# Optimization experiments

Measured on AMD Instinct MI355X. Metric: run time of the kernel, lower is better.

## Reference

```python
import jax, jax.numpy as jnp
import numpy as np

B, N, Q, H = 32, 1024, 64, 768


def setup_inputs() -> dict:
    key = jax.random.key(0)
    k1, k2, k3, k4 = jax.random.split(key, 4)
    return {
        "nodes_compress": jax.random.normal(k1, (B, N, H), dtype=jnp.float32),
        "query_compress": jax.random.normal(k2, (B, Q, H), dtype=jnp.float32),
        "nodes_hidden": jax.random.normal(k3, (B, N, H), dtype=jnp.float32),
        # nn.Linear(3H, 1, bias=False).weight flattened to (3H,)
        "w": jax.random.normal(k4, (3 * H,), dtype=jnp.float32) * (1.0 / np.sqrt(3 * H)),
    }


def reference(nodes_compress, query_compress, nodes_hidden, w):
    h = nodes_compress.shape[-1]
    w_n, w_q, w_nq = w[:h], w[h:2 * h], w[2 * h:]
    # Decomposed trilinear similarity: identical to Linear([n, q, n*q]) -> scalar
    sim = (
        (nodes_compress @ w_n)[:, :, None]          # (B, N, 1)
        + (query_compress @ w_q)[:, None, :]        # (B, 1, Q)
        + jnp.einsum("bnh,bqh,h->bnq", nodes_compress, query_compress, w_nq)
    )                                                # (B, N, Q)
    # nodes -> query attention
    a = jax.nn.softmax(sim, axis=-1)                 # (B, N, Q)
    nodes2query = jnp.einsum("bnq,bqh->bnh", a, query_compress)
    # query -> nodes attention (max over query, softmax over nodes)
    b = jax.nn.softmax(jnp.max(sim, axis=-1), axis=-1)  # (B, N)
    q2n = jnp.einsum("bn,bnh->bh", b, nodes_compress)[:, None, :]  # (B, 1, H)
    q2n = jnp.broadcast_to(q2n, nodes_compress.shape)               # (B, N, H)
    return jnp.concatenate(
        [nodes_compress, nodes2query, nodes_compress * nodes2query, nodes_compress * q2n],
        axis=-1,
    )  # (B, N, 4H)
```

## Files before the change

kernel.cpp:

```cpp
#include <hip/hip_runtime.h>
#include <hip/hip_bf16.h>

#define BB 32
#define NN 1024
#define QQ 64
#define HH 768

typedef __attribute__((ext_vector_type(8))) short short8;
typedef __attribute__((ext_vector_type(4))) float f32x4;

#define GLOAD_LDS16(gp, lp) \
  __builtin_amdgcn_global_load_lds((const __attribute__((address_space(1))) unsigned int*)(gp), \
                                   (__attribute__((address_space(3))) unsigned int*)(lp), 16, 0, 0)

__device__ __forceinline__ unsigned short f2b(float f) {
  unsigned int u = __float_as_uint(f);
  unsigned int r = u + 0x7fffu + ((u >> 16) & 1u);
  return (unsigned short)(r >> 16);
}

__global__ __launch_bounds__(256) void k_prep(
    const float* __restrict__ qc, const float* __restrict__ w,
    unsigned short* __restrict__ qwB, unsigned short* __restrict__ qcT,
    float* __restrict__ sq_part) {
  __shared__ float qcL[128][66];

  const int tid = threadIdx.x;
  const int bid = blockIdx.x;
  const int b = bid / 6, hc = bid % 6;
  const float* qcB = qc + (size_t)(b * 64) * HH + hc * 128;

#pragma unroll
  for (int i = 0; i < 8; ++i) {
    int u = i * 256 + tid;
    int q = u >> 5, c4 = u & 31;
    float4 v = *(const float4*)(qcB + (size_t)q * HH + c4 * 4);
    qcL[c4 * 4 + 0][q] = v.x;
    qcL[c4 * 4 + 1][q] = v.y;
    qcL[c4 * 4 + 2][q] = v.z;
    qcL[c4 * 4 + 3][q] = v.w;
  }
  __syncthreads();

  {
    char* dst = (char*)qwB + ((size_t)bid << 14);
#pragma unroll
    for (int i = 0; i < 4; ++i) {
      int p = i * 256 + tid;
      int q = p >> 4, uu = p & 15;
      int hg = hc * 128 + uu * 8;
      short8 v;
#pragma unroll
      for (int j = 0; j < 8; ++j)
        v[j] = (short)f2b(qcL[uu * 8 + j][q] * w[2 * HH + hg + j] + w[hg + j]);
      *(short8*)(dst + ((size_t)(q * 16 + (uu ^ (q & 7)))) * 16) = v;
    }
  }
  {
    char* dst = (char*)qcT + ((size_t)bid << 14);
#pragma unroll
    for (int i = 0; i < 4; ++i) {
      int p = i * 256 + tid;
      int r = p >> 3, x = p & 7;
      int xu = x ^ (r & 7);
      short8 v;
#pragma unroll
      for (int j = 0; j < 8; ++j) v[j] = (short)f2b(qcL[r][xu * 8 + j]);
      *(short8*)(dst + (size_t)p * 16) = v;
    }
  }
  {
    int q = tid >> 2, qt = tid & 3;
    float s = 0.f;
#pragma unroll
    for (int k = 0; k < 32; ++k)
      s += qcL[qt * 32 + k][q] * w[HH + hc * 128 + qt * 32 + k];
    s += __shfl_xor(s, 1);
    s += __shfl_xor(s, 2);
    if (qt == 0) sq_part[bid * 64 + q] = s;
  }
}

__global__ __launch_bounds__(256) void k_sim(
    const float* __restrict__ nc, const unsigned short* __restrict__ qwB,
    const float* __restrict__ sq_part, float* __restrict__ partial,
    float* __restrict__ mtse, unsigned short* __restrict__ probs)
{
  __shared__ __align__(16) char bbuf[2][16384];
  __shared__ float rowmF[64];
  __shared__ float wvF[64];
  __shared__ float pW[4][768];

  const int tid = threadIdx.x;
  const int wv_ = tid >> 6, l = tid & 63;
  const int l15 = l & 15, lg = l >> 4;
  const int lb = (blockIdx.x & 7) * 64 + (blockIdx.x >> 3);
  const int b = lb >> 4, tile = lb & 15;
  const int row0 = tile * 64;

  const float* ncB = nc + (size_t)(b * NN + row0) * HH;
  const char* qwb = (const char*)qwB + (size_t)b * 98304;
  const float* aBase = ncB + (wv_ * 16 + l15) * HH + lg * 8;

  {
    const char* gsrc = qwb + wv_ * 4096 + l * 16;
#pragma unroll
    for (int i = 0; i < 4; ++i)
      GLOAD_LDS16(gsrc + i * 1024, &bbuf[0][wv_ * 4096 + i * 1024]);
  }
  float4 fr[2][8];
#pragma unroll
  for (int ks = 0; ks < 4; ++ks) {
    fr[0][ks * 2]     = *(const float4*)(aBase + ks * 32);
    fr[0][ks * 2 + 1] = *(const float4*)(aBase + ks * 32 + 4);
  }

  f32x4 acc[4] = {};
#pragma unroll
  for (int kc = 0; kc < 6; ++kc) {
    short8 af[4];
#pragma unroll
    for (int ks = 0; ks < 4; ++ks) {
      float4 f0 = fr[kc & 1][ks * 2], f1 = fr[kc & 1][ks * 2 + 1];
      short8 v;
      v[0] = (short)f2b(f0.x); v[1] = (short)f2b(f0.y);
      v[2] = (short)f2b(f0.z); v[3] = (short)f2b(f0.w);
      v[4] = (short)f2b(f1.x); v[5] = (short)f2b(f1.y);
      v[6] = (short)f2b(f1.z); v[7] = (short)f2b(f1.w);
      af[ks] = v;
    }
    if (kc < 5) {
#pragma unroll
      for (int ks = 0; ks < 4; ++ks) {
        fr[(kc + 1) & 1][ks * 2]     = *(const float4*)(aBase + (kc + 1) * 128 + ks * 32);
        fr[(kc + 1) & 1][ks * 2 + 1] = *(const float4*)(aBase + (kc + 1) * 128 + ks * 32 + 4);
      }
      const char* gsrc = qwb + (kc + 1) * 16384 + wv_ * 4096 + l * 16;
#pragma unroll
      for (int i = 0; i < 4; ++i)
        GLOAD_LDS16(gsrc + i * 1024, &bbuf[(kc + 1) & 1][wv_ * 4096 + i * 1024]);
      asm volatile("s_waitcnt vmcnt(12)" ::: "memory");
    } else {
      asm volatile("s_waitcnt vmcnt(0)" ::: "memory");
    }
    __builtin_amdgcn_s_barrier();
    __builtin_amdgcn_sched_barrier(0);
#pragma unroll
    for (int ks = 0; ks < 4; ++ks) {
      int kbyte = ks * 64 + lg * 16;
#pragma unroll
      for (int nt = 0; nt < 4; ++nt) {
        int brow = nt * 16 + l15;
        short8 bf = *(short8*)(&bbuf[kc & 1][0] + brow * 256 + (kbyte ^ ((l & 7) << 4)));
        acc[nt] = __builtin_amdgcn_mfma_f32_16x16x32_bf16(af[ks], bf, acc[nt], 0, 0, 0);
      }
    }
    __builtin_amdgcn_sched_barrier(0);
    __builtin_amdgcn_s_barrier();
  }

  unsigned short* pT = probs + (size_t)(b * 16 + tile) * (QQ * QQ);
  float sqv[4];
#pragma unroll
  for (int nt = 0; nt < 4; ++nt) {
    float s = 0.f;
#pragma unroll
    for (int i = 0; i < 6; ++i) s += sq_part[(b * 6 + i) * 64 + nt * 16 + l15];
    sqv[nt] = s;
  }
#pragma unroll
  for (int j = 0; j < 4; ++j) {
    float mm = -1e30f;
#pragma unroll
    for (int nt = 0; nt < 4; ++nt) { acc[nt][j] += sqv[nt]; mm = fmaxf(mm, acc[nt][j]); }
    mm = fmaxf(mm, __shfl_xor(mm, 1));
    mm = fmaxf(mm, __shfl_xor(mm, 2));
    mm = fmaxf(mm, __shfl_xor(mm, 4));
    mm = fmaxf(mm, __shfl_xor(mm, 8));
    float ss = 0.f;
#pragma unroll
    for (int nt = 0; nt < 4; ++nt) { float p = __expf(acc[nt][j] - mm); acc[nt][j] = p; ss += p; }
    ss += __shfl_xor(ss, 1); ss += __shfl_xor(ss, 2);
    ss += __shfl_xor(ss, 4); ss += __shfl_xor(ss, 8);
    float inv = 1.0f / ss;
    int r = wv_ * 16 + lg * 4 + j;
#pragma unroll
    for (int nt = 0; nt < 4; ++nt)
      pT[r * 64 + nt * 16 + l15] = f2b(acc[nt][j] * inv);
    if (l15 == 0) rowmF[r] = mm;
  }
  __syncthreads();

  float m_t = -1e30f;
#pragma unroll
  for (int i = 0; i < 16; ++i) {
    f32x4 v = ((f32x4*)rowmF)[i];
    m_t = fmaxf(m_t, fmaxf(fmaxf(v[0], v[1]), fmaxf(v[2], v[3])));
  }
  if (tid < 64) wvF[tid] = __expf(rowmF[tid] - m_t);
  __syncthreads();
  {
    float sv = wvF[l];
#pragma unroll
    for (int m = 1; m < 64; m <<= 1) sv += __shfl_xor(sv, m);
    if (tid == 0) {
      mtse[(b * 16 + tile) * 2] = m_t;
      mtse[(b * 16 + tile) * 2 + 1] = sv;
    }
  }
  {
    float a[12];
#pragma unroll
    for (int j = 0; j < 12; ++j) a[j] = 0.f;
    for (int n0 = 0; n0 < 16; ++n0) {
      int n = wv_ * 16 + n0;
      float wvv = wvF[n];
      const float* pr = ncB + (size_t)n * HH;
#pragma unroll
      for (int j = 0; j < 12; ++j) a[j] += wvv * pr[l + j * 64];
    }
#pragma unroll
    for (int j = 0; j < 12; ++j) pW[wv_][l + j * 64] = a[j];
  }
  __syncthreads();
  {
    float* pp = partial + (size_t)(b * 16 + tile) * HH + tid;
    pp[0]   = pW[0][tid]       + pW[1][tid]       + pW[2][tid]       + pW[3][tid];
    pp[256] = pW[0][tid + 256] + pW[1][tid + 256] + pW[2][tid + 256] + pW[3][tid + 256];
    pp[512] = pW[0][tid + 512] + pW[1][tid + 512] + pW[2][tid + 512] + pW[3][tid + 512];
  }
}

__global__ __launch_bounds__(256) void k_out(
    const float* __restrict__ nc, const unsigned short* __restrict__ qcT,
    const unsigned short* __restrict__ probs, const float* __restrict__ partial,
    const float* __restrict__ mtse, float* __restrict__ out)
{
  __shared__ __align__(16) char smem[16384];
  __shared__ float q2nL[128];

  const int tid = threadIdx.x;
  const int wv_ = tid >> 6, l = tid & 63;
  const int l15 = l & 15, lg = l >> 4;
  const int lb = (blockIdx.x & 7) * 384 + (blockIdx.x >> 3);
  const int hc = lb % 6;
  const int bt = lb / 6;
  const int b = bt >> 4, tile = bt & 15;
  const int row0 = tile * 64;

  {
    const char* src = (const char*)qcT + ((size_t)(b * 6 + hc) << 14) + wv_ * 4096 + l * 16;
#pragma unroll
    for (int i = 0; i < 4; ++i)
      GLOAD_LDS16(src + i * 1024, &smem[wv_ * 4096 + i * 1024]);
  }

  if (tid < 128) {
    float M = -1e30f, mt[16], se[16];
#pragma unroll
    for (int i = 0; i < 16; ++i) {
      mt[i] = mtse[(b * 16 + i) * 2];
      se[i] = mtse[(b * 16 + i) * 2 + 1];
      M = fmaxf(M, mt[i]);
    }
    float denom = 0.f;
#pragma unroll
    for (int i = 0; i < 16; ++i) { mt[i] = __expf(mt[i] - M); denom += mt[i] * se[i]; }
    float inv = 1.0f / denom;
    float a = 0.f;
#pragma unroll
    for (int i = 0; i < 16; ++i)
      a += mt[i] * partial[(size_t)(b * 16 + i) * HH + hc * 128 + tid];
    q2nL[tid] = a * inv;
  }

  const unsigned short* pT = probs + (size_t)bt * (QQ * QQ);
  short8 a2_0 = *(const short8*)((const char*)pT + (wv_ * 16 + l15) * 128 + lg * 16);
  short8 a2_1 = *(const short8*)((const char*)pT + (wv_ * 16 + l15) * 128 + 64 + lg * 16);

  asm volatile("s_waitcnt vmcnt(0)" ::: "memory");
  __syncthreads();

  const int n = wv_ * 16 + l15;
  const float* ncrow = nc + (size_t)(b * NN + row0 + n) * HH;
  float* orow = out + (size_t)(b * NN + row0 + n) * 3072;

#pragma unroll
  for (int hg = 0; hg < 8; ++hg) {
    f32x4 c2 = {};
#pragma unroll
    for (int ks2 = 0; ks2 < 2; ++ks2) {
      int hrow = hg * 16 + l15;
      int kbyte = ks2 * 64 + lg * 16;
      short8 hf = *(short8*)(&smem[0] + hrow * 128 + (kbyte ^ ((l & 7) << 4)));
      c2 = __builtin_amdgcn_mfma_f32_16x16x32_bf16(hf, ks2 ? a2_1 : a2_0, c2, 0, 0, 0);
    }
    int hl = hg * 16 + lg * 4;
    int hbase = hc * 128 + hl;
    f32x4 ncv = *(const f32x4*)(ncrow + hbase);
    f32x4 qv  = *(const f32x4*)(&q2nL[hl]);
    *(f32x4*)(orow + hbase)          = ncv;
    *(f32x4*)(orow + HH + hbase)     = c2;
    *(f32x4*)(orow + 2 * HH + hbase) = ncv * c2;
    *(f32x4*)(orow + 2304 + hbase)   = ncv * qv;
  }
}

extern "C" void kernel_launch(void* const* d_in, const int* in_sizes, int n_in,
                              void* d_out, int out_size, void* d_ws, size_t ws_size,
                              hipStream_t stream) {
  (void)in_sizes; (void)n_in; (void)out_size; (void)ws_size;
  const float* nc = (const float*)d_in[0];
  const float* qc = (const float*)d_in[1];
  const float* w  = (const float*)d_in[3];
  float* out = (float*)d_out;
  char* ws = (char*)d_ws;
  unsigned short* qwB = (unsigned short*)(ws);
  unsigned short* qcT = (unsigned short*)(ws + 3145728);
  float* sq_part = (float*)(ws + 6291456);
  float* partial = (float*)(ws + 6340608);
  float* mtse    = (float*)(ws + 7913472);
  unsigned short* probs = (unsigned short*)(ws + 7917568);

  k_prep<<<192, 256, 0, stream>>>(qc, w, qwB, qcT, sq_part);
  k_sim<<<512, 256, 0, stream>>>(nc, qwB, sq_part, partial, mtse, probs);
  k_out<<<3072, 256, 0, stream>>>(nc, qcT, probs, partial, mtse, out);
}
```

Measured before the change: 158.7 us.

## Split similarity GEMM along H into two halves in a separate kernel

The fused sim+softmax kernel becomes two kernels. k_mm runs 1024 blocks, each computing half of the H reduction and writing a partial 64x64 fp32 sim tile to workspace. k_soft sums the two halves and runs the existing softmax and partial logic. This doubles the blocks for the GEMM phase, which improves occupancy and latency hiding. The cost is an extra kernel launch, a global round trip of the partial sims, and k_soft re-reading nodes_compress.

```diff
diff --git a/kernel.cpp b/kernel.cpp
--- a/kernel.cpp
+++ b/kernel.cpp
@@ -81,43 +81,39 @@
   }
 }
 
-__global__ __launch_bounds__(256) void k_sim(
+__global__ __launch_bounds__(256) void k_mm(
     const float* __restrict__ nc, const unsigned short* __restrict__ qwB,
-    const float* __restrict__ sq_part, float* __restrict__ partial,
-    float* __restrict__ mtse, unsigned short* __restrict__ probs)
+    float* __restrict__ simh)
 {
   __shared__ __align__(16) char bbuf[2][16384];
-  __shared__ float rowmF[64];
-  __shared__ float wvF[64];
-  __shared__ float pW[4][768];
 
   const int tid = threadIdx.x;
   const int wv_ = tid >> 6, l = tid & 63;
   const int l15 = l & 15, lg = l >> 4;
-  const int lb = (blockIdx.x & 7) * 64 + (blockIdx.x >> 3);
-  const int b = lb >> 4, tile = lb & 15;
+  const int lb = (blockIdx.x & 7) * 128 + (blockIdx.x >> 3);
+  const int b = lb >> 5, tile = (lb >> 1) & 15, kh = lb & 1;
   const int row0 = tile * 64;
 
   const float* ncB = nc + (size_t)(b * NN + row0) * HH;
-  const char* qwb = (const char*)qwB + (size_t)b * 98304;
-  const float* aBase = ncB + (wv_ * 16 + l15) * HH + lg * 8;
-
-  {
-    const char* gsrc = qwb + wv_ * 4096 + l * 16;
-#pragma unroll
-    for (int i = 0; i < 4; ++i)
-      GLOAD_LDS16(gsrc + i * 1024, &bbuf[0][wv_ * 4096 + i * 1024]);
-  }
+  const char* qwb = (const char*)qwB + (size_t)b * 98304 + (size_t)kh * 49152;
+  const float* aBase = ncB + (wv_ * 16 + l15) * HH + kh * 384 + lg * 8;
+
   float4 fr[2][8];
 #pragma unroll
   for (int ks = 0; ks < 4; ++ks) {
     fr[0][ks * 2]     = *(const float4*)(aBase + ks * 32);
     fr[0][ks * 2 + 1] = *(const float4*)(aBase + ks * 32 + 4);
   }
+  {
+    const char* gsrc = qwb + wv_ * 4096 + l * 16;
+#pragma unroll
+    for (int i = 0; i < 4; ++i)
+      GLOAD_LDS16(gsrc + i * 1024, &bbuf[0][wv_ * 4096 + i * 1024]);
+  }
 
   f32x4 acc[4] = {};
 #pragma unroll
-  for (int kc = 0; kc < 6; ++kc) {
+  for (int kc = 0; kc < 3; ++kc) {
     short8 af[4];
 #pragma unroll
     for (int ks = 0; ks < 4; ++ks) {
@@ -129,7 +125,7 @@
       v[6] = (short)f2b(f1.z); v[7] = (short)f2b(f1.w);
       af[ks] = v;
     }
-    if (kc < 5) {
+    if (kc < 2) {
 #pragma unroll
       for (int ks = 0; ks < 4; ++ks) {
         fr[(kc + 1) & 1][ks * 2]     = *(const float4*)(aBase + (kc + 1) * 128 + ks * 32);
@@ -156,10 +152,38 @@
       }
     }
     __builtin_amdgcn_sched_barrier(0);
-    __builtin_amdgcn_s_barrier();
-  }
-
-  unsigned short* pT = probs + (size_t)(b * 16 + tile) * (QQ * QQ);
+    if (kc == 0) __builtin_amdgcn_s_barrier();
+  }
+
+  float* sh = simh + ((size_t)((b * 16 + tile) * 2 + kh)) * 4096;
+#pragma unroll
+  for (int nt = 0; nt < 4; ++nt)
+#pragma unroll
+    for (int j = 0; j < 4; ++j)
+      sh[(wv_ * 16 + lg * 4 + j) * 64 + nt * 16 + l15] = acc[nt][j];
+}
+
+__global__ __launch_bounds__(256) void k_soft(
+    const float* __restrict__ nc, const float* __restrict__ simh,
+    const float* __restrict__ sq_part, float* __restrict__ partial,
+    float* __restrict__ mtse, unsigned short* __restrict__ probs)
+{
+  __shared__ float rowmF[64];
+  __shared__ float wvF[64];
+  __shared__ float pW[4][768];
+
+  const int tid = threadIdx.x;
+  const int wv_ = tid >> 6, l = tid & 63;
+  const int l15 = l & 15, lg = l >> 4;
+  const int lb = (blockIdx.x & 7) * 64 + (blockIdx.x >> 3);
+  const int b = lb >> 4, tile = lb & 15;
+  const int row0 = tile * 64;
+
+  const float* ncB = nc + (size_t)(b * NN + row0) * HH;
+  const float* sh0 = simh + ((size_t)((b * 16 + tile) * 2)) * 4096;
+  const float* sh1 = sh0 + 4096;
+
+  f32x4 acc[4];
   float sqv[4];
 #pragma unroll
   for (int nt = 0; nt < 4; ++nt) {
@@ -167,7 +191,14 @@
 #pragma unroll
     for (int i = 0; i < 6; ++i) s += sq_part[(b * 6 + i) * 64 + nt * 16 + l15];
     sqv[nt] = s;
-  }
+#pragma unroll
+    for (int j = 0; j < 4; ++j) {
+      int idx = (wv_ * 16 + lg * 4 + j) * 64 + nt * 16 + l15;
+      acc[nt][j] = sh0[idx] + sh1[idx];
+    }
+  }
+
+  unsigned short* pT = probs + (size_t)(b * 16 + tile) * (QQ * QQ);
 #pragma unroll
   for (int j = 0; j < 4; ++j) {
     float mm = -1e30f;
@@ -321,8 +352,10 @@
   float* partial = (float*)(ws + 6340608);
   float* mtse    = (float*)(ws + 7913472);
   unsigned short* probs = (unsigned short*)(ws + 7917568);
+  float* simh    = (float*)(ws + 12111872);
 
   k_prep<<<192, 256, 0, stream>>>(qc, w, qwB, qcT, sq_part);
-  k_sim<<<512, 256, 0, stream>>>(nc, qwB, sq_part, partial, mtse, probs);
+  k_mm<<<1024, 256, 0, stream>>>(nc, qwB, simh);
+  k_soft<<<512, 256, 0, stream>>>(nc, simh, sq_part, partial, mtse, probs);
   k_out<<<3072, 256, 0, stream>>>(nc, qcT, probs, partial, mtse, out);
 }
```

New measurement: 174.7 us. +10.1%, slower.
